# Kernel optimization log

Hardware: AMD Instinct MI355X
Metric: run time of the kernel (lower is better)

Reference implementation:

```python
import jax, jax.numpy as jnp
import numpy as np

# Llama-3-8B-ish config + NSA defaults from the adapter
H, KVH, DH = 32, 8, 128
D = H * DH            # 4096 hidden
CB = 16               # compress block size (stride == block -> non-overlapping)
SB = 16               # selection block size
NSEL = 4              # num selected blocks
WIN = 64              # sliding window size
B, S = 1, 1024
NEG = -jnp.finfo(jnp.float32).max


def rope(x):
    # interleaved rotary (rotary_embedding_torch default, theta=10000); x: [b,h,n,d]
    b, h, n, d = x.shape
    inv = 1.0 / (10000.0 ** (jnp.arange(0, d, 2, dtype=jnp.float32) / d))
    ang = jnp.arange(n, dtype=jnp.float32)[:, None] * inv[None, :]      # [n, d/2]
    cos, sin = jnp.cos(ang), jnp.sin(ang)
    xr = x.reshape(b, h, n, d // 2, 2)
    x0, x1 = xr[..., 0], xr[..., 1]
    o0 = x0 * cos - x1 * sin
    o1 = x1 * cos + x0 * sin
    return jnp.stack([o0, o1], axis=-1).reshape(b, h, n, d)


def nsa_forward(hidden_states, w_qkv, w_o, k_pos, v_pos,
                k_w1, k_b1, k_w2, k_b2, v_w1, v_b1, v_w2, v_b2,
                mem_kv, w_gate, b_gate):
    Bq, Sq = hidden_states.shape[:2]
    G = H // KVH
    scale = DH ** -0.5

    qkv = hidden_states @ w_qkv.T
    q, k, v = jnp.split(qkv, [H * DH, H * DH + KVH * DH], axis=-1)
    q = q.reshape(Bq, Sq, H, DH).transpose(0, 2, 1, 3)     # b h s d
    k = k.reshape(Bq, Sq, KVH, DH).transpose(0, 2, 1, 3)   # b kvh s d
    v = v.reshape(Bq, Sq, KVH, DH).transpose(0, 2, 1, 3)

    # ---- branch 1: compressed (coarse) attention ------------------------
    nC = Sq // CB
    kp = jnp.tile(k_pos, (1, nC, 1))[None]                 # intra-block learned positions
    vp = jnp.tile(v_pos, (1, nC, 1))[None]
    ck_in = (k + kp).reshape(Bq, KVH, nC, CB * DH)
    cv_in = (v + vp).reshape(Bq, KVH, nC, CB * DH)
    ck = jax.nn.relu(ck_in @ k_w1.T + k_b1) @ k_w2.T + k_b2   # b kvh nC d
    cv = jax.nn.relu(cv_in @ v_w1.T + v_b1) @ v_w2.T + v_b2
    mem_k = jnp.broadcast_to(mem_kv[0], (Bq, KVH, 1, DH))
    mem_v = jnp.broadcast_to(mem_kv[1], (Bq, KVH, 1, DH))
    ck = jnp.concatenate([mem_k, ck], axis=2)              # b kvh (1+nC) d
    cv = jnp.concatenate([mem_v, cv], axis=2)

    qg = q.reshape(Bq, KVH, G, Sq, DH)
    csim = jnp.einsum('bhgid,bhjd->bhgij', qg, ck) * scale
    ck_seq = jnp.concatenate([jnp.array([-1]), (jnp.arange(nC) + 1) * CB - 1])
    cmask = ck_seq[None, :] < jnp.arange(Sq)[:, None]      # [S, 1+nC], mem always visible
    csim = jnp.where(cmask, csim, NEG)
    c_out = jnp.einsum('bhgij,bhjd->bhgid', jax.nn.softmax(csim, -1), cv)
    c_out = c_out.reshape(Bq, H, Sq, DH)

    # ---- importance scores -> top-k selected blocks ---------------------
    imp = csim[..., 1:].mean(axis=2)                       # mean over grouped q heads: b kvh s nC
    sent = jnp.full(imp.shape[:-1] + (1,), -1e3, imp.dtype)
    imp = jax.nn.softmax(jnp.concatenate([sent, imp], -1), -1)[..., 1:]
    sel_val, sel_idx = jax.lax.top_k(imp, NSEL)            # b kvh s NSEL
    fmask_sel = sel_val > 1e-10

    rq, rk = rope(q), rope(k)

    # ---- branch 2: fine attention over selected + own (block-causal) block
    own = jnp.arange(Sq) // SB
    sel_idx = jnp.concatenate(
        [sel_idx, jnp.broadcast_to(own, (Bq, KVH, Sq))[..., None]], axis=-1)  # b kvh s (NSEL+1)
    nF = Sq // SB
    fk_b = rk.reshape(Bq, KVH, nF, SB, DH)
    fv_b = v.reshape(Bq, KVH, nF, SB, DH)
    bi = jnp.arange(Bq)[:, None, None, None]
    hi = jnp.arange(KVH)[None, :, None, None]
    fk = fk_b[bi, hi, sel_idx].reshape(Bq, KVH, Sq, (NSEL + 1) * SB, DH)
    fv = fv_b[bi, hi, sel_idx].reshape(Bq, KVH, Sq, (NSEL + 1) * SB, DH)

    diag = jnp.arange(SB)[None, :] <= (jnp.arange(Sq) % SB)[:, None]   # [S, SB]
    fmask = jnp.concatenate(
        [jnp.broadcast_to(fmask_sel[..., None], (Bq, KVH, Sq, NSEL, SB)),
         jnp.broadcast_to(diag, (Bq, KVH, Sq, SB))[..., None, :]], axis=3)
    fmask = fmask.reshape(Bq, KVH, 1, Sq, (NSEL + 1) * SB)

    fq = rq.reshape(Bq, KVH, G, Sq, DH)
    fsim = jnp.einsum('bhgid,bhijd->bhgij', fq, fk) * scale
    fsim = jnp.where(fmask, fsim, NEG)
    f_out = jnp.einsum('bhgij,bhijd->bhgid', jax.nn.softmax(fsim, -1), fv)
    f_out = f_out.reshape(Bq, H, Sq, DH)

    # ---- branch 3: sliding window (exact window, look_backward=1) -------
    sk = jnp.repeat(rk, G, axis=1)                          # b H s d
    sv = jnp.repeat(v, G, axis=1)
    nW = Sq // WIN
    sqw = rq.reshape(Bq, H, nW, WIN, DH)
    skw = sk.reshape(Bq, H, nW, WIN, DH)
    svw = sv.reshape(Bq, H, nW, WIN, DH)
    pad5 = ((0, 0), (0, 0), (1, 0), (0, 0), (0, 0))
    skc = jnp.concatenate([jnp.pad(skw, pad5)[:, :, :nW], skw], axis=3)  # prev + own window
    svc = jnp.concatenate([jnp.pad(svw, pad5)[:, :, :nW], svw], axis=3)
    rel = (WIN + jnp.arange(WIN))[:, None] - jnp.arange(2 * WIN)[None, :]  # i_abs - j_abs
    band = (rel >= 0) & (rel <= WIN)
    key_abs = jnp.arange(nW)[:, None] * WIN + jnp.arange(2 * WIN)[None, :] - WIN
    smask = band[None] & (key_abs >= 0)[:, None, :]
    ssim = jnp.einsum('bhwid,bhwjd->bhwij', sqw, skc) * scale
    ssim = jnp.where(smask, ssim, NEG)
    s_out = jnp.einsum('bhwij,bhwjd->bhwid', jax.nn.softmax(ssim, -1), svc)
    s_out = s_out.reshape(Bq, H, Sq, DH)

    # ---- learned 3-way gate + output projection --------------------------
    gates = jax.nn.sigmoid(hidden_states @ w_gate.T + b_gate)
    gates = gates.reshape(Bq, Sq, H, 3).transpose(0, 2, 1, 3)  # b h s 3
    out = gates[..., 0:1] * c_out + gates[..., 1:2] * f_out + gates[..., 2:3] * s_out
    out = out.transpose(0, 2, 1, 3).reshape(Bq, Sq, H * DH)
    return out @ w_o.T


def setup_inputs():
    key = jax.random.key(0)
    ks = jax.random.split(key, 12)
    cdim = CB * DH
    rn = lambda k, shape, s: jax.random.normal(k, shape, dtype=jnp.float32) * s
    return {
        'hidden_states': rn(ks[0], (B, S, D), 1.0),
        'w_qkv': rn(ks[1], (H * DH + 2 * KVH * DH, D), D ** -0.5),
        'w_o': rn(ks[2], (D, H * DH), D ** -0.5),
        'k_pos': rn(ks[3], (KVH, CB, DH), 0.02),
        'v_pos': rn(ks[4], (KVH, CB, DH), 0.02),
        'k_w1': rn(ks[5], (cdim, cdim), cdim ** -0.5),
        'k_b1': jnp.zeros((cdim,), jnp.float32),
        'k_w2': rn(ks[6], (DH, cdim), cdim ** -0.5),
        'k_b2': jnp.zeros((DH,), jnp.float32),
        'v_w1': rn(ks[7], (cdim, cdim), cdim ** -0.5),
        'v_b1': jnp.zeros((cdim,), jnp.float32),
        'v_w2': rn(ks[8], (DH, cdim), cdim ** -0.5),
        'v_b2': jnp.zeros((DH,), jnp.float32),
        'mem_kv': rn(ks[9], (2, KVH, 1, DH), 0.02),
        'w_gate': rn(ks[10], (3 * H, D), 0.02),
        'b_gate': jnp.tile(jnp.array([-2.0, -2.0, 2.0], jnp.float32), H),
    }


def reference(hidden_states, w_qkv, w_o, k_pos, v_pos,
              k_w1, k_b1, k_w2, k_b2, v_w1, v_b1, v_w2, v_b2,
              mem_kv, w_gate, b_gate):
    return nsa_forward(hidden_states, w_qkv, w_o, k_pos, v_pos,
                       k_w1, k_b1, k_w2, k_b2, v_w1, v_b1, v_w2, v_b2,
                       mem_kv, w_gate, b_gate)
```

## Files before the change

### kernel.cpp

```cpp
#include <hip/hip_runtime.h>
#include <hip/hip_bf16.h>

typedef __hip_bfloat16 bf16;
typedef __attribute__((ext_vector_type(8))) short short8;
typedef __attribute__((ext_vector_type(4))) float f32x4;

#define NEGF (-3.402823466e38f)
#define SCALE 0.08838834764831845f

constexpr int S_    = 1024;
constexpr int H_    = 32;
constexpr int KVH_  = 8;
constexpr int DH_   = 128;
constexpr int QKVN  = 6144;
constexpr int NC_   = 64;
constexpr int CD_   = 2048;

__device__ __forceinline__ short f2bf(float x) {
    union { float f; unsigned u; } v; v.f = x;
    unsigned r = v.u + 0x7fffu + ((v.u >> 16) & 1u);
    return (short)(r >> 16);
}
__device__ __forceinline__ float bf2f(short h) {
    union { float f; unsigned u; } v; v.u = ((unsigned)(unsigned short)h) << 16;
    return v.f;
}

#define GLOAD16(gp, lp) __builtin_amdgcn_global_load_lds( \
    (const __attribute__((address_space(1))) unsigned int*)(gp), \
    (__attribute__((address_space(3))) unsigned int*)(lp), 16, 0, 0)

__global__ void split_pair(const float* __restrict__ src, short* __restrict__ h,
                           short* __restrict__ l, long n)
{
    long i = ((long)blockIdx.x * blockDim.x + threadIdx.x) * 8;
    if (i >= n) return;
    float4 a0 = *(const float4*)&src[i];
    float4 a1 = *(const float4*)&src[i + 4];
    float e[8] = {a0.x, a0.y, a0.z, a0.w, a1.x, a1.y, a1.z, a1.w};
    short8 hh, ll;
    #pragma unroll
    for (int j = 0; j < 8; ++j) {
        short hv = f2bf(e[j]); hh[j] = hv; ll[j] = f2bf(e[j] - bf2f(hv));
    }
    *(short8*)&h[i] = hh;
    *(short8*)&l[i] = ll;
}

__global__ __launch_bounds__(256)
void gemm_bf3(const short* __restrict__ Ah, const short* __restrict__ Al,
              const short* __restrict__ Bh, const short* __restrict__ Bl,
              float* __restrict__ C, float* __restrict__ Cpart,
              const float* __restrict__ bias,
              int M, int N, int K, int ldc, int k_len, int act)
{
    __shared__ short LAh[2][4096];
    __shared__ short LAl[2][4096];
    __shared__ short LBh[2][4096];
    __shared__ short LBl[2][4096];
    const int tid  = threadIdx.x;
    const int lane = tid & 63, wave = tid >> 6;
    const int wr = wave >> 1, wc = wave & 1;
    const int qd = lane >> 4, l16 = lane & 15;
    const int bm = blockIdx.y * 128, bn = blockIdx.x * 128;
    const int kbeg = blockIdx.z * k_len;
    const int kend = kbeg + k_len;

    const short* gA[2][2];
    const short* gB[2][2];
    int cbase[2];
    #pragma unroll
    for (int c = 0; c < 2; ++c) {
        int cell = (wave * 2 + c) * 64 + lane;
        int row = cell & 127, kq = cell >> 7;
        size_t oa = (size_t)(bm + row) * K + kq * 8;
        size_t ob = (size_t)(bn + row) * K + kq * 8;
        gA[c][0] = Ah + oa; gA[c][1] = Al + oa;
        gB[c][0] = Bh + ob; gB[c][1] = Bl + ob;
        cbase[c] = (wave * 2 + c) * 512;
    }

    #define STAGE(buf, kk) do {                          \
        _Pragma("unroll")                                \
        for (int c = 0; c < 2; ++c) {                    \
            GLOAD16(gA[c][0] + (kk), &LAh[buf][cbase[c]]); \
            GLOAD16(gA[c][1] + (kk), &LAl[buf][cbase[c]]); \
            GLOAD16(gB[c][0] + (kk), &LBh[buf][cbase[c]]); \
            GLOAD16(gB[c][1] + (kk), &LBl[buf][cbase[c]]); \
        } } while (0)

    f32x4 zero = {0.f, 0.f, 0.f, 0.f};
    f32x4 acc[4][4];
    #pragma unroll
    for (int i = 0; i < 4; ++i)
        #pragma unroll
        for (int j = 0; j < 4; ++j) acc[i][j] = zero;

    STAGE(0, kbeg);
    int cur = 0;
    for (int k0 = kbeg; k0 < kend; k0 += 32) {
        bool hasnext = (k0 + 32) < kend;
        if (hasnext) {
            STAGE(cur ^ 1, k0 + 32);
            asm volatile("s_waitcnt vmcnt(8)" ::: "memory");
        } else {
            asm volatile("s_waitcnt vmcnt(0)" ::: "memory");
        }
        __builtin_amdgcn_s_barrier();

        short8 fah[4], fal[4], fbh[4], fbl[4];
        #pragma unroll
        for (int t = 0; t < 4; ++t) {
            int ca = (qd * 128 + wr * 64 + t * 16 + l16) * 8;
            int cb = (qd * 128 + wc * 64 + t * 16 + l16) * 8;
            fah[t] = *(const short8*)&LAh[cur][ca]; fal[t] = *(const short8*)&LAl[cur][ca];
            fbh[t] = *(const short8*)&LBh[cur][cb]; fbl[t] = *(const short8*)&LBl[cur][cb];
        }
        #pragma unroll
        for (int i = 0; i < 4; ++i)
            #pragma unroll
            for (int j = 0; j < 4; ++j) {
                acc[i][j] = __builtin_amdgcn_mfma_f32_16x16x32_bf16(fah[i], fbh[j], acc[i][j], 0, 0, 0);
                acc[i][j] = __builtin_amdgcn_mfma_f32_16x16x32_bf16(fah[i], fbl[j], acc[i][j], 0, 0, 0);
                acc[i][j] = __builtin_amdgcn_mfma_f32_16x16x32_bf16(fal[i], fbh[j], acc[i][j], 0, 0, 0);
            }
        asm volatile("s_waitcnt lgkmcnt(0)" ::: "memory");
        __builtin_amdgcn_s_barrier();
        cur ^= 1;
    }
    #undef STAGE

    float* dst = Cpart ? (Cpart + (size_t)blockIdx.z * M * ldc) : C;
    #pragma unroll
    for (int i = 0; i < 4; ++i) {
        #pragma unroll
        for (int j = 0; j < 4; ++j) {
            int row0 = bm + wr * 64 + i * 16 + qd * 4;
            int col  = bn + wc * 64 + j * 16 + l16;
            #pragma unroll
            for (int r = 0; r < 4; ++r) {
                float v = acc[i][j][r];
                if (!Cpart) {
                    if (bias) v += bias[col];
                    if (act == 1) v = fmaxf(v, 0.f);
                    else if (act == 2) v = 1.f / (1.f + expf(-v));
                }
                dst[(size_t)(row0 + r) * ldc + col] = v;
            }
        }
    }
}

__global__ __launch_bounds__(256)
void gemm128(const float* __restrict__ A, const float* __restrict__ B,
             float* __restrict__ C, float* __restrict__ Cpart,
             const float* __restrict__ bias,
             int M, int N, int K, int k_len, int act)
{
    __shared__ float As[16][132];
    __shared__ float Bs[16][132];
    const int tid  = threadIdx.x;
    const int wave = tid >> 6, lane = tid & 63;
    const int wr = wave >> 1, wc = wave & 1;
    const int ro = wr * 64 + (lane >> 3) * 8;
    const int co = wc * 64 + (lane & 7) * 8;
    const int bm = blockIdx.y * 128, bn = blockIdx.x * 128;
    const int z  = blockIdx.z;
    const int kbeg = z * k_len;
    const int lr = tid >> 2;
    const int kq = (tid & 3) * 4;

    float acc[8][8];
    #pragma unroll
    for (int i = 0; i < 8; ++i)
        #pragma unroll
        for (int j = 0; j < 8; ++j) acc[i][j] = 0.f;

    for (int k0 = kbeg; k0 < kbeg + k_len; k0 += 16) {
        #pragma unroll
        for (int h = 0; h < 2; ++h) {
            int r = lr + h * 64;
            float4 av = make_float4(0.f, 0.f, 0.f, 0.f);
            float4 bv = make_float4(0.f, 0.f, 0.f, 0.f);
            if (bm + r < M) av = *(const float4*)&A[(size_t)(bm + r) * K + k0 + kq];
            if (bn + r < N) bv = *(const float4*)&B[(size_t)(bn + r) * K + k0 + kq];
            As[kq + 0][r] = av.x; As[kq + 1][r] = av.y;
            As[kq + 2][r] = av.z; As[kq + 3][r] = av.w;
            Bs[kq + 0][r] = bv.x; Bs[kq + 1][r] = bv.y;
            Bs[kq + 2][r] = bv.z; Bs[kq + 3][r] = bv.w;
        }
        __syncthreads();
        #pragma unroll
        for (int kk = 0; kk < 16; ++kk) {
            float4 a0 = *(const float4*)&As[kk][ro];
            float4 a1 = *(const float4*)&As[kk][ro + 4];
            float4 b0 = *(const float4*)&Bs[kk][co];
            float4 b1 = *(const float4*)&Bs[kk][co + 4];
            float a[8] = {a0.x, a0.y, a0.z, a0.w, a1.x, a1.y, a1.z, a1.w};
            float b[8] = {b0.x, b0.y, b0.z, b0.w, b1.x, b1.y, b1.z, b1.w};
            #pragma unroll
            for (int i = 0; i < 8; ++i)
                #pragma unroll
                for (int j = 0; j < 8; ++j)
                    acc[i][j] += a[i] * b[j];
        }
        __syncthreads();
    }

    if (Cpart) {
        float* P = Cpart + (size_t)z * M * N;
        #pragma unroll
        for (int i = 0; i < 8; ++i) {
            int row = bm + ro + i;
            #pragma unroll
            for (int jq = 0; jq < 2; ++jq) {
                int col = bn + co + jq * 4;
                if (col < N) {
                    float4 v = make_float4(acc[i][jq * 4 + 0], acc[i][jq * 4 + 1],
                                           acc[i][jq * 4 + 2], acc[i][jq * 4 + 3]);
                    *(float4*)&P[(size_t)row * N + col] = v;
                }
            }
        }
    } else {
        #pragma unroll
        for (int i = 0; i < 8; ++i) {
            int row = bm + ro + i;
            #pragma unroll
            for (int jq = 0; jq < 2; ++jq) {
                int col = bn + co + jq * 4;
                if (col < N) {
                    float4 v = make_float4(acc[i][jq * 4 + 0], acc[i][jq * 4 + 1],
                                           acc[i][jq * 4 + 2], acc[i][jq * 4 + 3]);
                    if (bias) {
                        float4 bv = *(const float4*)&bias[col];
                        v.x += bv.x; v.y += bv.y; v.z += bv.z; v.w += bv.w;
                    }
                    if (act == 1) {
                        v.x = fmaxf(v.x, 0.f); v.y = fmaxf(v.y, 0.f);
                        v.z = fmaxf(v.z, 0.f); v.w = fmaxf(v.w, 0.f);
                    } else if (act == 2) {
                        v.x = 1.f / (1.f + expf(-v.x)); v.y = 1.f / (1.f + expf(-v.y));
                        v.z = 1.f / (1.f + expf(-v.z)); v.w = 1.f / (1.f + expf(-v.w));
                    }
                    *(float4*)&C[(size_t)row * N + col] = v;
                }
            }
        }
    }
}

__global__ void reduce_slices(const float* __restrict__ P, float* __restrict__ C,
                              const float* __restrict__ bias,
                              int MN, int N, int KS, int act)
{
    int i4 = blockIdx.x * blockDim.x + threadIdx.x;
    size_t base = (size_t)i4 * 4;
    if (base >= (size_t)MN) return;
    float4 s = *(const float4*)&P[base];
    for (int z = 1; z < KS; ++z) {
        float4 v = *(const float4*)&P[(size_t)z * MN + base];
        s.x += v.x; s.y += v.y; s.z += v.z; s.w += v.w;
    }
    if (bias) {
        int col = (int)(base % N);
        float4 bv = *(const float4*)&bias[col];
        s.x += bv.x; s.y += bv.y; s.z += bv.z; s.w += bv.w;
    }
    if (act == 1) {
        s.x = fmaxf(s.x, 0.f); s.y = fmaxf(s.y, 0.f);
        s.z = fmaxf(s.z, 0.f); s.w = fmaxf(s.w, 0.f);
    } else if (act == 2) {
        s.x = 1.f / (1.f + expf(-s.x)); s.y = 1.f / (1.f + expf(-s.y));
        s.z = 1.f / (1.f + expf(-s.z)); s.w = 1.f / (1.f + expf(-s.w));
    }
    *(float4*)&C[base] = s;
}

__global__ void build_cin(const float* __restrict__ qkv,
                          const float* __restrict__ k_pos,
                          const float* __restrict__ v_pos,
                          short* __restrict__ ckh, short* __restrict__ ckl,
                          short* __restrict__ cvh, short* __restrict__ cvl)
{
    int idx = blockIdx.x * blockDim.x + threadIdx.x;
    if (idx >= KVH_ * S_ * DH_) return;
    int d = idx & 127;
    int s = (idx >> 7) & 1023;
    int h = idx >> 17;
    int c = s >> 4, t = s & 15;
    float kv = qkv[(size_t)s * QKVN + 4096 + h * DH_ + d];
    float vv = qkv[(size_t)s * QKVN + 5120 + h * DH_ + d];
    size_t row = (size_t)h * NC_ + c;
    size_t col = (size_t)t * DH_ + d;
    float kx = kv + k_pos[(h * 16 + t) * DH_ + d];
    float vx = vv + v_pos[(h * 16 + t) * DH_ + d];
    short kh = f2bf(kx), vh = f2bf(vx);
    ckh[row * CD_ + col] = kh; ckl[row * CD_ + col] = f2bf(kx - bf2f(kh));
    cvh[row * CD_ + col] = vh; cvl[row * CD_ + col] = f2bf(vx - bf2f(vh));
}

__global__ void assemble_c(const float* __restrict__ ckb, const float* __restrict__ cvb,
                           const float* __restrict__ mem_kv,
                           float* __restrict__ ckf, float* __restrict__ cvf)
{
    int idx = blockIdx.x * blockDim.x + threadIdx.x;
    if (idx >= KVH_ * 65 * DH_) return;
    int d = idx & 127;
    int j = (idx >> 7) % 65;
    int h = idx / (65 * DH_);
    if (j == 0) {
        ckf[idx] = mem_kv[(0 * KVH_ + h) * DH_ + d];
        cvf[idx] = mem_kv[(1 * KVH_ + h) * DH_ + d];
    } else {
        ckf[idx] = ckb[((size_t)h * NC_ + (j - 1)) * DH_ + d];
        cvf[idx] = cvb[((size_t)h * NC_ + (j - 1)) * DH_ + d];
    }
}

__global__ void compress_attn(const float* __restrict__ qkv,
                              const float* __restrict__ ckf,
                              const float* __restrict__ cvf,
                              float* __restrict__ cout,
                              int* __restrict__ selidx, int* __restrict__ fsel)
{
    int b = blockIdx.x;
    int s = b & 1023;
    int h = b >> 10;
    int tid = threadIdx.x;
    int wv = tid >> 6;
    __shared__ __align__(16) float qrow[4][128];
    __shared__ float simS[4][65];
    __shared__ float p[4][128];
    __shared__ float redm[2][4], redd[2][4];
    #pragma unroll
    for (int g = 0; g < 4; ++g)
        qrow[g][tid] = qkv[(size_t)s * QKVN + (h * 4 + g) * DH_ + tid];
    __syncthreads();

    float sv[4] = {NEGF, NEGF, NEGF, NEGF};
    if (tid < 65) {
        bool vis = (tid == 0) || (16 * tid - 1 < s);
        if (vis) {
            const float4* kr = (const float4*)(ckf + ((size_t)h * 65 + tid) * DH_);
            float a[4] = {0.f, 0.f, 0.f, 0.f};
            #pragma unroll 4
            for (int d = 0; d < 32; ++d) {
                float4 kq = kr[d];
                #pragma unroll
                for (int g = 0; g < 4; ++g) {
                    float4 qq = *(const float4*)&qrow[g][d * 4];
                    a[g] += kq.x * qq.x + kq.y * qq.y + kq.z * qq.z + kq.w * qq.w;
                }
            }
            #pragma unroll
            for (int g = 0; g < 4; ++g) sv[g] = a[g] * SCALE;
        }
        #pragma unroll
        for (int g = 0; g < 4; ++g) simS[g][tid] = sv[g];
    }

    float mg[4];
    #pragma unroll
    for (int g = 0; g < 4; ++g) mg[g] = sv[g];
    #pragma unroll
    for (int off = 32; off; off >>= 1)
        #pragma unroll
        for (int g = 0; g < 4; ++g) mg[g] = fmaxf(mg[g], __shfl_xor(mg[g], off));
    if ((tid & 63) == 0)
        #pragma unroll
        for (int g = 0; g < 4; ++g) redm[wv][g] = mg[g];
    __syncthreads();
    float e[4];
    #pragma unroll
    for (int g = 0; g < 4; ++g) {
        float m = fmaxf(redm[0][g], redm[1][g]);
        e[g] = (tid < 65) ? expf(sv[g] - m) : 0.f;
        p[g][tid] = e[g];
    }
    __syncthreads();
    #pragma unroll
    for (int off = 32; off; off >>= 1)
        #pragma unroll
        for (int g = 0; g < 4; ++g) e[g] += __shfl_xor(e[g], off);
    if ((tid & 63) == 0)
        #pragma unroll
        for (int g = 0; g < 4; ++g) redd[wv][g] = e[g];
    __syncthreads();
    float inv[4];
    #pragma unroll
    for (int g = 0; g < 4; ++g) inv[g] = 1.f / (redd[0][g] + redd[1][g]);

    if (wv == 1) {
        int j = tid - 64;
        float v = 0.25f * (simS[0][j + 1] + simS[1][j + 1] +
                           simS[2][j + 1] + simS[3][j + 1]);
        float m2 = v;
        #pragma unroll
        for (int off = 32; off; off >>= 1) m2 = fmaxf(m2, __shfl_xor(m2, off));
        m2 = fmaxf(m2, -1e3f);
        float e2 = expf(v - m2);
        float den2 = e2;
        #pragma unroll
        for (int off = 32; off; off >>= 1) den2 += __shfl_xor(den2, off);
        den2 += expf(-1e3f - m2);
        float pv = e2 / den2;
        size_t base5 = ((size_t)h * S_ + s) * 5;
        size_t base4 = ((size_t)h * S_ + s) * 4;
        float cv = pv; int ci = j;
        for (int t = 0; t < 4; ++t) {
            float bv = cv; int bi = ci;
            #pragma unroll
            for (int off = 32; off; off >>= 1) {
                float ov = __shfl_xor(bv, off);
                int   oi = __shfl_xor(bi, off);
                if (ov > bv || (ov == bv && oi < bi)) { bv = ov; bi = oi; }
            }
            if (j == 0) {
                selidx[base5 + t] = bi;
                fsel[base4 + t]   = (bv > 1e-10f) ? 1 : 0;
            }
            if (ci == bi) cv = -1.f;
        }
        if (j == 0) selidx[base5 + 4] = s >> 4;
    }

    float acc[4] = {0.f, 0.f, 0.f, 0.f};
    const float* vbase = cvf + (size_t)h * 65 * DH_ + tid;
    #pragma unroll 4
    for (int j = 0; j < 65; ++j) {
        float v = vbase[(size_t)j * DH_];
        #pragma unroll
        for (int g = 0; g < 4; ++g) acc[g] += p[g][j] * v;
    }
    #pragma unroll
    for (int g = 0; g < 4; ++g)
        cout[(size_t)s * 4096 + (h * 4 + g) * DH_ + tid] = acc[g] * inv[g];
}

__global__ void rope_inplace(float* __restrict__ qkv)
{
    int idx = blockIdx.x * blockDim.x + threadIdx.x;
    const int totq = S_ * H_ * 64;
    const int totk = S_ * KVH_ * 64;
    float* base;
    int p, s;
    if (idx < totq) {
        p = idx & 63; int head = (idx >> 6) & 31; s = idx >> 11;
        base = qkv + (size_t)s * QKVN + head * DH_;
    } else {
        int i2 = idx - totq;
        if (i2 >= totk) return;
        p = i2 & 63; int head = (i2 >> 6) & 7; s = i2 >> 9;
        base = qkv + (size_t)s * QKVN + 4096 + head * DH_;
    }
    float inv = exp2f(-0.2076205060833595f * (float)p);
    float ang = (float)s * inv;
    float c = cosf(ang), sn = sinf(ang);
    float x0 = base[2 * p], x1 = base[2 * p + 1];
    base[2 * p]     = x0 * c - x1 * sn;
    base[2 * p + 1] = x1 * c + x0 * sn;
}

__global__ void fine_attn(const float* __restrict__ qkv,
                          const int* __restrict__ selidx, const int* __restrict__ fsel,
                          float* __restrict__ fout)
{
    int b = blockIdx.x;
    int s = b & 1023;
    int h = b >> 10;
    int tid = threadIdx.x;
    int wv = tid >> 6;
    __shared__ __align__(16) float qrow[4][128];
    __shared__ float p[4][128];
    __shared__ int   blk[5];
    __shared__ int   bvis[5];
    __shared__ float redm[2][4], redd[2][4];
    if (tid < 5) {
        blk[tid]  = selidx[((size_t)h * S_ + s) * 5 + tid];
        bvis[tid] = (tid < 4) ? fsel[((size_t)h * S_ + s) * 4 + tid] : 1;
    }
    #pragma unroll
    for (int g = 0; g < 4; ++g)
        qrow[g][tid] = qkv[(size_t)s * QKVN + (h * 4 + g) * DH_ + tid];
    __syncthreads();

    float sv[4] = {NEGF, NEGF, NEGF, NEGF};
    if (tid < 80) {
        int bi = tid >> 4, t = tid & 15;
        int pos = blk[bi] * 16 + t;
        bool vis = (bi < 4) ? (bvis[bi] != 0) : (t <= (s & 15));
        if (vis) {
            const float4* kr = (const float4*)(qkv + (size_t)pos * QKVN + 4096 + h * DH_);
            float a[4] = {0.f, 0.f, 0.f, 0.f};
            #pragma unroll 4
            for (int d = 0; d < 32; ++d) {
                float4 kq = kr[d];
                #pragma unroll
                for (int g = 0; g < 4; ++g) {
                    float4 qq = *(const float4*)&qrow[g][d * 4];
                    a[g] += kq.x * qq.x + kq.y * qq.y + kq.z * qq.z + kq.w * qq.w;
                }
            }
            #pragma unroll
            for (int g = 0; g < 4; ++g) sv[g] = a[g] * SCALE;
        }
    }

    float mg[4];
    #pragma unroll
    for (int g = 0; g < 4; ++g) mg[g] = sv[g];
    #pragma unroll
    for (int off = 32; off; off >>= 1)
        #pragma unroll
        for (int g = 0; g < 4; ++g) mg[g] = fmaxf(mg[g], __shfl_xor(mg[g], off));
    if ((tid & 63) == 0)
        #pragma unroll
        for (int g = 0; g < 4; ++g) redm[wv][g] = mg[g];
    __syncthreads();
    float e[4];
    #pragma unroll
    for (int g = 0; g < 4; ++g) {
        float m = fmaxf(redm[0][g], redm[1][g]);
        e[g] = (tid < 80) ? expf(sv[g] - m) : 0.f;
        p[g][tid] = e[g];
    }
    __syncthreads();
    #pragma unroll
    for (int off = 32; off; off >>= 1)
        #pragma unroll
        for (int g = 0; g < 4; ++g) e[g] += __shfl_xor(e[g], off);
    if ((tid & 63) == 0)
        #pragma unroll
        for (int g = 0; g < 4; ++g) redd[wv][g] = e[g];
    __syncthreads();
    float inv[4];
    #pragma unroll
    for (int g = 0; g < 4; ++g) inv[g] = 1.f / (redd[0][g] + redd[1][g]);

    float acc[4] = {0.f, 0.f, 0.f, 0.f};
    const float* vbase = qkv + 5120 + h * DH_ + tid;
    #pragma unroll
    for (int bi = 0; bi < 5; ++bi) {
        const float* vb = vbase + (size_t)(blk[bi] * 16) * QKVN;
        #pragma unroll 4
        for (int t = 0; t < 16; ++t) {
            float v = vb[(size_t)t * QKVN];
            #pragma unroll
            for (int g = 0; g < 4; ++g) acc[g] += p[g][bi * 16 + t] * v;
        }
    }
    #pragma unroll
    for (int g = 0; g < 4; ++g)
        fout[(size_t)s * 4096 + (h * 4 + g) * DH_ + tid] = acc[g] * inv[g];
}

__global__ void sliding_attn(const float* __restrict__ qkv, float* __restrict__ sout)
{
    int b = blockIdx.x;
    int s = b & 1023;
    int h = b >> 10;
    int tid = threadIdx.x;
    int wv = tid >> 6;
    __shared__ __align__(16) float qrow[4][128];
    __shared__ float p[4][128];
    __shared__ float redm[2][4], redd[2][4];
    #pragma unroll
    for (int g = 0; g < 4; ++g)
        qrow[g][tid] = qkv[(size_t)s * QKVN + (h * 4 + g) * DH_ + tid];
    __syncthreads();

    float sv[4] = {NEGF, NEGF, NEGF, NEGF};
    if (tid < 65) {
        int pos = s - tid;
        if (pos >= 0) {
            const float4* kr = (const float4*)(qkv + (size_t)pos * QKVN + 4096 + h * DH_);
            float a[4] = {0.f, 0.f, 0.f, 0.f};
            #pragma unroll 4
            for (int d = 0; d < 32; ++d) {
                float4 kq = kr[d];
                #pragma unroll
                for (int g = 0; g < 4; ++g) {
                    float4 qq = *(const float4*)&qrow[g][d * 4];
                    a[g] += kq.x * qq.x + kq.y * qq.y + kq.z * qq.z + kq.w * qq.w;
                }
            }
            #pragma unroll
            for (int g = 0; g < 4; ++g) sv[g] = a[g] * SCALE;
        }
    }

    float mg[4];
    #pragma unroll
    for (int g = 0; g < 4; ++g) mg[g] = sv[g];
    #pragma unroll
    for (int off = 32; off; off >>= 1)
        #pragma unroll
        for (int g = 0; g < 4; ++g) mg[g] = fmaxf(mg[g], __shfl_xor(mg[g], off));
    if ((tid & 63) == 0)
        #pragma unroll
        for (int g = 0; g < 4; ++g) redm[wv][g] = mg[g];
    __syncthreads();
    float e[4];
    #pragma unroll
    for (int g = 0; g < 4; ++g) {
        float m = fmaxf(redm[0][g], redm[1][g]);
        e[g] = (tid < 65) ? expf(sv[g] - m) : 0.f;
        p[g][tid] = e[g];
    }
    __syncthreads();
    #pragma unroll
    for (int off = 32; off; off >>= 1)
        #pragma unroll
        for (int g = 0; g < 4; ++g) e[g] += __shfl_xor(e[g], off);
    if ((tid & 63) == 0)
        #pragma unroll
        for (int g = 0; g < 4; ++g) redd[wv][g] = e[g];
    __syncthreads();
    float inv[4];
    #pragma unroll
    for (int g = 0; g < 4; ++g) inv[g] = 1.f / (redd[0][g] + redd[1][g]);

    float acc[4] = {0.f, 0.f, 0.f, 0.f};
    int lim = (s + 1 < 65) ? (s + 1) : 65;
    const float* vbase = qkv + (size_t)s * QKVN + 5120 + h * DH_ + tid;
    #pragma unroll 4
    for (int j = 0; j < lim; ++j) {
        float v = *(vbase - (size_t)j * QKVN);
        #pragma unroll
        for (int g = 0; g < 4; ++g) acc[g] += p[g][j] * v;
    }
    #pragma unroll
    for (int g = 0; g < 4; ++g)
        sout[(size_t)s * 4096 + (h * 4 + g) * DH_ + tid] = acc[g] * inv[g];
}

__global__ void combine_gate(const float* __restrict__ cout, const float* __restrict__ fout,
                             const float* __restrict__ sout, const float* __restrict__ gates,
                             short* __restrict__ oh, short* __restrict__ ol)
{
    int idx = blockIdx.x * blockDim.x + threadIdx.x;
    if (idx >= S_ * 4096) return;
    int h = (idx >> 7) & 31;
    int s = idx >> 12;
    float g0 = gates[(size_t)s * 96 + h * 3 + 0];
    float g1 = gates[(size_t)s * 96 + h * 3 + 1];
    float g2 = gates[(size_t)s * 96 + h * 3 + 2];
    float v = g0 * cout[idx] + g1 * fout[idx] + g2 * sout[idx];
    short hv = f2bf(v);
    oh[idx] = hv;
    ol[idx] = f2bf(v - bf2f(hv));
}

extern "C" void kernel_launch(void* const* d_in, const int* in_sizes, int n_in,
                              void* d_out, int out_size, void* d_ws, size_t ws_size,
                              hipStream_t stream)
{
    const float* hidden = (const float*)d_in[0];
    const float* w_qkv  = (const float*)d_in[1];
    const float* w_o    = (const float*)d_in[2];
    const float* k_pos  = (const float*)d_in[3];
    const float* v_pos  = (const float*)d_in[4];
    const float* k_w1   = (const float*)d_in[5];
    const float* k_b1   = (const float*)d_in[6];
    const float* k_w2   = (const float*)d_in[7];
    const float* k_b2   = (const float*)d_in[8];
    const float* v_w1   = (const float*)d_in[9];
    const float* v_b1   = (const float*)d_in[10];
    const float* v_w2   = (const float*)d_in[11];
    const float* v_b2   = (const float*)d_in[12];
    const float* mem_kv = (const float*)d_in[13];
    const float* w_gate = (const float*)d_in[14];
    const float* b_gate = (const float*)d_in[15];
    float* out = (float*)d_out;

    float* ws = (float*)d_ws;
    size_t o = 0;
    float* qkv    = ws + o; o += (size_t)S_ * QKVN;
    short* ckin_h = (short*)(ws + o); o += (size_t)512 * CD_ / 2;
    short* ckin_l = (short*)(ws + o); o += (size_t)512 * CD_ / 2;
    short* cvin_h = (short*)(ws + o); o += (size_t)512 * CD_ / 2;
    short* cvin_l = (short*)(ws + o); o += (size_t)512 * CD_ / 2;
    float* h1     = ws + o; o += (size_t)512 * CD_;
    float* ckb    = ws + o; o += (size_t)512 * DH_;
    float* cvb    = ws + o; o += (size_t)512 * DH_;
    float* ckf    = ws + o; o += (size_t)KVH_ * 65 * DH_;
    float* cvf    = ws + o; o += (size_t)KVH_ * 65 * DH_;
    float* coutb  = ws + o; o += (size_t)S_ * 4096;
    float* foutb  = ws + o; o += (size_t)S_ * 4096;
    float* soutb  = ws + o; o += (size_t)S_ * 4096;
    float* gatesb = ws + o; o += (size_t)S_ * 96;
    int*   selidx = (int*)(ws + o); o += (size_t)KVH_ * S_ * 5;
    int*   fsel   = (int*)(ws + o); o += (size_t)KVH_ * S_ * 4;
    short* hid_h  = (short*)(ws + o); o += (size_t)S_ * 4096 / 2;
    short* hid_l  = (short*)(ws + o); o += (size_t)S_ * 4096 / 2;
    short* cmb_h  = (short*)(ws + o); o += (size_t)S_ * 4096 / 2;
    short* cmb_l  = (short*)(ws + o); o += (size_t)S_ * 4096 / 2;
    short* wsp_h  = (short*)(ws + o); o += (size_t)QKVN * 4096 / 2;
    short* wsp_l  = (short*)(ws + o); o += (size_t)QKVN * 4096 / 2;

    float* P = foutb;

    {
        long n = (long)S_ * 4096;
        split_pair<<<(int)((n / 8 + 255) / 256), 256, 0, stream>>>(hidden, hid_h, hid_l, n);
        long nw = (long)QKVN * 4096;
        split_pair<<<(int)((nw / 8 + 255) / 256), 256, 0, stream>>>(w_qkv, wsp_h, wsp_l, nw);
    }

    gemm_bf3<<<dim3(QKVN / 128, S_ / 128, 1), 256, 0, stream>>>(
        hid_h, hid_l, wsp_h, wsp_l, qkv, nullptr, nullptr,
        S_, QKVN, 4096, QKVN, 4096, 0);

    gemm128<<<dim3(1, S_ / 128, 16), 256, 0, stream>>>(
        hidden, w_gate, nullptr, P, nullptr, S_, 96, 4096, 256, 0);
    reduce_slices<<<(S_ * 96 / 4 + 255) / 256, 256, 0, stream>>>(
        P, gatesb, b_gate, S_ * 96, 96, 16, 2);

    build_cin<<<(KVH_ * S_ * DH_ + 255) / 256, 256, 0, stream>>>(
        qkv, k_pos, v_pos, ckin_h, ckin_l, cvin_h, cvin_l);

    {
        long nw = (long)CD_ * CD_;
        split_pair<<<(int)((nw / 8 + 255) / 256), 256, 0, stream>>>(k_w1, wsp_h, wsp_l, nw);
    }
    gemm_bf3<<<dim3(CD_ / 128, 4, 8), 256, 0, stream>>>(
        ckin_h, ckin_l, wsp_h, wsp_l, nullptr, P, nullptr,
        512, CD_, CD_, CD_, 256, 0);
    reduce_slices<<<(512 * CD_ / 4 + 255) / 256, 256, 0, stream>>>(
        P, h1, k_b1, 512 * CD_, CD_, 8, 1);
    gemm128<<<dim3(1, 4, 16), 256, 0, stream>>>(
        h1, k_w2, nullptr, P, nullptr, 512, DH_, CD_, 128, 0);
    reduce_slices<<<(512 * DH_ / 4 + 255) / 256, 256, 0, stream>>>(
        P, ckb, k_b2, 512 * DH_, DH_, 16, 0);

    {
        long nw = (long)CD_ * CD_;
        split_pair<<<(int)((nw / 8 + 255) / 256), 256, 0, stream>>>(v_w1, wsp_h, wsp_l, nw);
    }
    gemm_bf3<<<dim3(CD_ / 128, 4, 8), 256, 0, stream>>>(
        cvin_h, cvin_l, wsp_h, wsp_l, nullptr, P, nullptr,
        512, CD_, CD_, CD_, 256, 0);
    reduce_slices<<<(512 * CD_ / 4 + 255) / 256, 256, 0, stream>>>(
        P, h1, v_b1, 512 * CD_, CD_, 8, 1);
    gemm128<<<dim3(1, 4, 16), 256, 0, stream>>>(
        h1, v_w2, nullptr, P, nullptr, 512, DH_, CD_, 128, 0);
    reduce_slices<<<(512 * DH_ / 4 + 255) / 256, 256, 0, stream>>>(
        P, cvb, v_b2, 512 * DH_, DH_, 16, 0);

    assemble_c<<<(KVH_ * 65 * DH_ + 255) / 256, 256, 0, stream>>>(ckb, cvb, mem_kv, ckf, cvf);

    compress_attn<<<KVH_ * S_, 128, 0, stream>>>(qkv, ckf, cvf, coutb, selidx, fsel);

    {
        int tot = S_ * H_ * 64 + S_ * KVH_ * 64;
        rope_inplace<<<(tot + 255) / 256, 256, 0, stream>>>(qkv);
    }

    fine_attn<<<KVH_ * S_, 128, 0, stream>>>(qkv, selidx, fsel, foutb);

    sliding_attn<<<KVH_ * S_, 128, 0, stream>>>(qkv, soutb);

    combine_gate<<<(S_ * 4096 + 255) / 256, 256, 0, stream>>>(
        coutb, foutb, soutb, gatesb, cmb_h, cmb_l);

    {
        long nw = (long)4096 * 4096;
        split_pair<<<(int)((nw / 8 + 255) / 256), 256, 0, stream>>>(w_o, wsp_h, wsp_l, nw);
    }
    gemm_bf3<<<dim3(4096 / 128, S_ / 128, 2), 256, 0, stream>>>(
        cmb_h, cmb_l, wsp_h, wsp_l, nullptr, P, nullptr,
        S_, 4096, 4096, 4096, 2048, 0);
    reduce_slices<<<(S_ * 4096 / 4 + 255) / 256, 256, 0, stream>>>(
        P, out, nullptr, S_ * 4096, 4096, 2, 0);
}
```

Baseline: 1.095 ms.

## Replace 128x128 bf16x3 GEMM with single-wave 64x64 barrier-free tile kernel

Swaps the four-wave 128x128 split-bf16 MFMA GEMM for a one-wave 64x64-tile kernel that needs no workgroup barriers and raises MFMA issue priority. It also moves the small second compression-MLP layer from the fp32 gemm128 onto this split-bf16 MFMA path, with the preceding reduce emitting hi/lo bf16 directly. The output projection drops its split-K partial-plus-reduce step. The cost is lower LDS reuse per block and more global loads per FLOP, plus a different occupancy profile.

```diff
diff --git a/kernel.cpp b/kernel.cpp
--- a/kernel.cpp
+++ b/kernel.cpp
@@ -47,46 +47,35 @@
     *(short8*)&l[i] = ll;
 }
 
-__global__ __launch_bounds__(256)
-void gemm_bf3(const short* __restrict__ Ah, const short* __restrict__ Al,
+__global__ __launch_bounds__(64)
+void gemm_w64(const short* __restrict__ Ah, const short* __restrict__ Al,
               const short* __restrict__ Bh, const short* __restrict__ Bl,
               float* __restrict__ C, float* __restrict__ Cpart,
               const float* __restrict__ bias,
               int M, int N, int K, int ldc, int k_len, int act)
 {
-    __shared__ short LAh[2][4096];
-    __shared__ short LAl[2][4096];
-    __shared__ short LBh[2][4096];
-    __shared__ short LBl[2][4096];
-    const int tid  = threadIdx.x;
-    const int lane = tid & 63, wave = tid >> 6;
-    const int wr = wave >> 1, wc = wave & 1;
+    __shared__ short LA[2][2][2048];
+    __shared__ short LB[2][2][2048];
+    const int lane = threadIdx.x;
     const int qd = lane >> 4, l16 = lane & 15;
-    const int bm = blockIdx.y * 128, bn = blockIdx.x * 128;
+    const int bm = blockIdx.y * 64, bn = blockIdx.x * 64;
     const int kbeg = blockIdx.z * k_len;
-    const int kend = kbeg + k_len;
-
-    const short* gA[2][2];
-    const short* gB[2][2];
-    int cbase[2];
-    #pragma unroll
-    for (int c = 0; c < 2; ++c) {
-        int cell = (wave * 2 + c) * 64 + lane;
-        int row = cell & 127, kq = cell >> 7;
-        size_t oa = (size_t)(bm + row) * K + kq * 8;
-        size_t ob = (size_t)(bn + row) * K + kq * 8;
-        gA[c][0] = Ah + oa; gA[c][1] = Al + oa;
-        gB[c][0] = Bh + ob; gB[c][1] = Bl + ob;
-        cbase[c] = (wave * 2 + c) * 512;
-    }
-
-    #define STAGE(buf, kk) do {                          \
-        _Pragma("unroll")                                \
-        for (int c = 0; c < 2; ++c) {                    \
-            GLOAD16(gA[c][0] + (kk), &LAh[buf][cbase[c]]); \
-            GLOAD16(gA[c][1] + (kk), &LAl[buf][cbase[c]]); \
-            GLOAD16(gB[c][0] + (kk), &LBh[buf][cbase[c]]); \
-            GLOAD16(gB[c][1] + (kk), &LBl[buf][cbase[c]]); \
+    const int kend = (kbeg + k_len < K) ? (kbeg + k_len) : K;
+
+    const int srow = lane >> 2, skq = lane & 3;
+    const short* gAh = Ah + (size_t)(bm + srow) * K + skq * 8;
+    const short* gAl = Al + (size_t)(bm + srow) * K + skq * 8;
+    const short* gBh = Bh + (size_t)(bn + srow) * K + skq * 8;
+    const short* gBl = Bl + (size_t)(bn + srow) * K + skq * 8;
+
+    #define STAGE(buf, kk) do {                                         \
+        _Pragma("unroll")                                               \
+        for (int c = 0; c < 4; ++c) {                                   \
+            size_t go = (size_t)c * 16 * K + (kk);                      \
+            GLOAD16(gAh + go, &LA[buf][0][c * 512]);                    \
+            GLOAD16(gAl + go, &LA[buf][1][c * 512]);                    \
+            GLOAD16(gBh + go, &LB[buf][0][c * 512]);                    \
+            GLOAD16(gBl + go, &LB[buf][1][c * 512]);                    \
         } } while (0)
 
     f32x4 zero = {0.f, 0.f, 0.f, 0.f};
@@ -99,47 +88,45 @@
     STAGE(0, kbeg);
     int cur = 0;
     for (int k0 = kbeg; k0 < kend; k0 += 32) {
-        bool hasnext = (k0 + 32) < kend;
-        if (hasnext) {
+        if (k0 + 32 < kend) {
             STAGE(cur ^ 1, k0 + 32);
-            asm volatile("s_waitcnt vmcnt(8)" ::: "memory");
+            asm volatile("s_waitcnt vmcnt(16)" ::: "memory");
         } else {
             asm volatile("s_waitcnt vmcnt(0)" ::: "memory");
         }
-        __builtin_amdgcn_s_barrier();
-
         short8 fah[4], fal[4], fbh[4], fbl[4];
         #pragma unroll
         for (int t = 0; t < 4; ++t) {
-            int ca = (qd * 128 + wr * 64 + t * 16 + l16) * 8;
-            int cb = (qd * 128 + wc * 64 + t * 16 + l16) * 8;
-            fah[t] = *(const short8*)&LAh[cur][ca]; fal[t] = *(const short8*)&LAl[cur][ca];
-            fbh[t] = *(const short8*)&LBh[cur][cb]; fbl[t] = *(const short8*)&LBl[cur][cb];
-        }
-        #pragma unroll
-        for (int i = 0; i < 4; ++i)
-            #pragma unroll
-            for (int j = 0; j < 4; ++j) {
-                acc[i][j] = __builtin_amdgcn_mfma_f32_16x16x32_bf16(fah[i], fbh[j], acc[i][j], 0, 0, 0);
-                acc[i][j] = __builtin_amdgcn_mfma_f32_16x16x32_bf16(fah[i], fbl[j], acc[i][j], 0, 0, 0);
-                acc[i][j] = __builtin_amdgcn_mfma_f32_16x16x32_bf16(fal[i], fbh[j], acc[i][j], 0, 0, 0);
-            }
-        asm volatile("s_waitcnt lgkmcnt(0)" ::: "memory");
-        __builtin_amdgcn_s_barrier();
+            int off = t * 512 + l16 * 32 + qd * 8;
+            fah[t] = *(const short8*)&LA[cur][0][off];
+            fal[t] = *(const short8*)&LA[cur][1][off];
+            fbh[t] = *(const short8*)&LB[cur][0][off];
+            fbl[t] = *(const short8*)&LB[cur][1][off];
+        }
+        __builtin_amdgcn_s_setprio(1);
+        #pragma unroll
+        for (int t = 0; t < 4; ++t)
+            #pragma unroll
+            for (int u = 0; u < 4; ++u) {
+                acc[t][u] = __builtin_amdgcn_mfma_f32_16x16x32_bf16(fah[t], fbh[u], acc[t][u], 0, 0, 0);
+                acc[t][u] = __builtin_amdgcn_mfma_f32_16x16x32_bf16(fah[t], fbl[u], acc[t][u], 0, 0, 0);
+                acc[t][u] = __builtin_amdgcn_mfma_f32_16x16x32_bf16(fal[t], fbh[u], acc[t][u], 0, 0, 0);
+            }
+        __builtin_amdgcn_s_setprio(0);
         cur ^= 1;
     }
     #undef STAGE
 
     float* dst = Cpart ? (Cpart + (size_t)blockIdx.z * M * ldc) : C;
     #pragma unroll
-    for (int i = 0; i < 4; ++i) {
-        #pragma unroll
-        for (int j = 0; j < 4; ++j) {
-            int row0 = bm + wr * 64 + i * 16 + qd * 4;
-            int col  = bn + wc * 64 + j * 16 + l16;
+    for (int t = 0; t < 4; ++t) {
+        #pragma unroll
+        for (int u = 0; u < 4; ++u) {
+            int row0 = bm + t * 16 + qd * 4;
+            int col  = bn + u * 16 + l16;
             #pragma unroll
             for (int r = 0; r < 4; ++r) {
-                float v = acc[i][j][r];
+                float v = acc[t][u][r];
                 if (!Cpart) {
                     if (bias) v += bias[col];
                     if (act == 1) v = fmaxf(v, 0.f);
@@ -251,6 +238,7 @@
 }
 
 __global__ void reduce_slices(const float* __restrict__ P, float* __restrict__ C,
+                              short* __restrict__ Chi, short* __restrict__ Clo,
                               const float* __restrict__ bias,
                               int MN, int N, int KS, int act)
 {
@@ -274,7 +262,18 @@
         s.x = 1.f / (1.f + expf(-s.x)); s.y = 1.f / (1.f + expf(-s.y));
         s.z = 1.f / (1.f + expf(-s.z)); s.w = 1.f / (1.f + expf(-s.w));
     }
-    *(float4*)&C[base] = s;
+    if (Chi) {
+        float e[4] = {s.x, s.y, s.z, s.w};
+        short4 hh, ll;
+        hh.x = f2bf(e[0]); ll.x = f2bf(e[0] - bf2f(hh.x));
+        hh.y = f2bf(e[1]); ll.y = f2bf(e[1] - bf2f(hh.y));
+        hh.z = f2bf(e[2]); ll.z = f2bf(e[2] - bf2f(hh.z));
+        hh.w = f2bf(e[3]); ll.w = f2bf(e[3] - bf2f(hh.w));
+        *(short4*)&Chi[base] = hh;
+        *(short4*)&Clo[base] = ll;
+    } else {
+        *(float4*)&C[base] = s;
+    }
 }
 
 __global__ void build_cin(const float* __restrict__ qkv,
@@ -681,7 +680,8 @@
     short* ckin_l = (short*)(ws + o); o += (size_t)512 * CD_ / 2;
     short* cvin_h = (short*)(ws + o); o += (size_t)512 * CD_ / 2;
     short* cvin_l = (short*)(ws + o); o += (size_t)512 * CD_ / 2;
-    float* h1     = ws + o; o += (size_t)512 * CD_;
+    short* h1h    = (short*)(ws + o); o += (size_t)512 * CD_ / 2;
+    short* h1l    = (short*)(ws + o); o += (size_t)512 * CD_ / 2;
     float* ckb    = ws + o; o += (size_t)512 * DH_;
     float* cvb    = ws + o; o += (size_t)512 * DH_;
     float* ckf    = ws + o; o += (size_t)KVH_ * 65 * DH_;
@@ -708,14 +708,14 @@
         split_pair<<<(int)((nw / 8 + 255) / 256), 256, 0, stream>>>(w_qkv, wsp_h, wsp_l, nw);
     }
 
-    gemm_bf3<<<dim3(QKVN / 128, S_ / 128, 1), 256, 0, stream>>>(
+    gemm_w64<<<dim3(QKVN / 64, S_ / 64, 1), 64, 0, stream>>>(
         hid_h, hid_l, wsp_h, wsp_l, qkv, nullptr, nullptr,
         S_, QKVN, 4096, QKVN, 4096, 0);
 
     gemm128<<<dim3(1, S_ / 128, 16), 256, 0, stream>>>(
         hidden, w_gate, nullptr, P, nullptr, S_, 96, 4096, 256, 0);
     reduce_slices<<<(S_ * 96 / 4 + 255) / 256, 256, 0, stream>>>(
-        P, gatesb, b_gate, S_ * 96, 96, 16, 2);
+        P, gatesb, nullptr, nullptr, b_gate, S_ * 96, 96, 16, 2);
 
     build_cin<<<(KVH_ * S_ * DH_ + 255) / 256, 256, 0, stream>>>(
         qkv, k_pos, v_pos, ckin_h, ckin_l, cvin_h, cvin_l);
@@ -724,29 +724,39 @@
         long nw = (long)CD_ * CD_;
         split_pair<<<(int)((nw / 8 + 255) / 256), 256, 0, stream>>>(k_w1, wsp_h, wsp_l, nw);
     }
-    gemm_bf3<<<dim3(CD_ / 128, 4, 8), 256, 0, stream>>>(
+    gemm_w64<<<dim3(CD_ / 64, 8, 4), 64, 0, stream>>>(
         ckin_h, ckin_l, wsp_h, wsp_l, nullptr, P, nullptr,
-        512, CD_, CD_, CD_, 256, 0);
+        512, CD_, CD_, CD_, 512, 0);
     reduce_slices<<<(512 * CD_ / 4 + 255) / 256, 256, 0, stream>>>(
-        P, h1, k_b1, 512 * CD_, CD_, 8, 1);
-    gemm128<<<dim3(1, 4, 16), 256, 0, stream>>>(
-        h1, k_w2, nullptr, P, nullptr, 512, DH_, CD_, 128, 0);
+        P, nullptr, h1h, h1l, k_b1, 512 * CD_, CD_, 4, 1);
+    {
+        long nw = (long)DH_ * CD_;
+        split_pair<<<(int)((nw / 8 + 255) / 256), 256, 0, stream>>>(k_w2, wsp_h, wsp_l, nw);
+    }
+    gemm_w64<<<dim3(DH_ / 64, 8, 16), 64, 0, stream>>>(
+        h1h, h1l, wsp_h, wsp_l, nullptr, P, nullptr,
+        512, DH_, CD_, DH_, 128, 0);
     reduce_slices<<<(512 * DH_ / 4 + 255) / 256, 256, 0, stream>>>(
-        P, ckb, k_b2, 512 * DH_, DH_, 16, 0);
+        P, ckb, nullptr, nullptr, k_b2, 512 * DH_, DH_, 16, 0);
 
     {
         long nw = (long)CD_ * CD_;
         split_pair<<<(int)((nw / 8 + 255) / 256), 256, 0, stream>>>(v_w1, wsp_h, wsp_l, nw);
     }
-    gemm_bf3<<<dim3(CD_ / 128, 4, 8), 256, 0, stream>>>(
+    gemm_w64<<<dim3(CD_ / 64, 8, 4), 64, 0, stream>>>(
         cvin_h, cvin_l, wsp_h, wsp_l, nullptr, P, nullptr,
-        512, CD_, CD_, CD_, 256, 0);
+        512, CD_, CD_, CD_, 512, 0);
     reduce_slices<<<(512 * CD_ / 4 + 255) / 256, 256, 0, stream>>>(
-        P, h1, v_b1, 512 * CD_, CD_, 8, 1);
-    gemm128<<<dim3(1, 4, 16), 256, 0, stream>>>(
-        h1, v_w2, nullptr, P, nullptr, 512, DH_, CD_, 128, 0);
+        P, nullptr, h1h, h1l, v_b1, 512 * CD_, CD_, 4, 1);
+    {
+        long nw = (long)DH_ * CD_;
+        split_pair<<<(int)((nw / 8 + 255) / 256), 256, 0, stream>>>(v_w2, wsp_h, wsp_l, nw);
+    }
+    gemm_w64<<<dim3(DH_ / 64, 8, 16), 64, 0, stream>>>(
+        h1h, h1l, wsp_h, wsp_l, nullptr, P, nullptr,
+        512, DH_, CD_, DH_, 128, 0);
     reduce_slices<<<(512 * DH_ / 4 + 255) / 256, 256, 0, stream>>>(
-        P, cvb, v_b2, 512 * DH_, DH_, 16, 0);
+        P, cvb, nullptr, nullptr, v_b2, 512 * DH_, DH_, 16, 0);
 
     assemble_c<<<(KVH_ * 65 * DH_ + 255) / 256, 256, 0, stream>>>(ckb, cvb, mem_kv, ckf, cvf);
 
@@ -768,9 +778,7 @@
         long nw = (long)4096 * 4096;
         split_pair<<<(int)((nw / 8 + 255) / 256), 256, 0, stream>>>(w_o, wsp_h, wsp_l, nw);
     }
-    gemm_bf3<<<dim3(4096 / 128, S_ / 128, 2), 256, 0, stream>>>(
-        cmb_h, cmb_l, wsp_h, wsp_l, nullptr, P, nullptr,
-        S_, 4096, 4096, 4096, 2048, 0);
-    reduce_slices<<<(S_ * 4096 / 4 + 255) / 256, 256, 0, stream>>>(
-        P, out, nullptr, S_ * 4096, 4096, 2, 0);
-}
+    gemm_w64<<<dim3(4096 / 64, S_ / 64, 1), 64, 0, stream>>>(
+        cmb_h, cmb_l, wsp_h, wsp_l, out, nullptr, nullptr,
+        S_, 4096, 4096, 4096, 4096, 0);
+}
```

Result: faster. 1.060 ms (-3.2%).
